# Kernel tuning notes

Hardware: AMD Instinct MI355X
Metric: run time of the kernel (lower is better)

The kernel has to match this reference:

```python
import jax, jax.numpy as jnp
import numpy as np

D_IN = 1024
D_OUT = 1024

def setup_inputs() -> dict:
    key = jax.random.key(0)
    ks = jax.random.split(key, 7)
    s = 1.0 / np.sqrt(D_IN)
    x = jax.random.normal(ks[0], (4, 2048, D_IN), dtype=jnp.float32)
    Wq = jax.random.uniform(ks[1], (D_IN, D_OUT), jnp.float32, -s, s)
    bq = jax.random.uniform(ks[2], (D_OUT,), jnp.float32, -s, s)
    Wk = jax.random.uniform(ks[3], (D_IN, D_OUT), jnp.float32, -s, s)
    bk = jax.random.uniform(ks[4], (D_OUT,), jnp.float32, -s, s)
    Wv = jax.random.uniform(ks[5], (D_IN, D_OUT), jnp.float32, -s, s)
    bv = jax.random.uniform(ks[6], (D_OUT,), jnp.float32, -s, s)
    return {"x": x, "Wq": Wq, "bq": bq, "Wk": Wk, "bk": bk, "Wv": Wv, "bv": bv}

def reference(x, Wq, bq, Wk, bk, Wv, bv):
    # q,k,v: [B, T, d_out]
    q = x @ Wq + bq
    k = x @ Wk + bk
    v = x @ Wv + bv
    T = x.shape[1]
    scale = 1.0 / jnp.sqrt(jnp.asarray(D_OUT, x.dtype))
    qk = jnp.einsum('btd,bsd->bts', q, k) * scale  # [B, T, T]
    causal = jnp.tril(jnp.ones((T, T), dtype=bool))
    qk = jnp.where(causal, qk, -jnp.inf)
    probs = jax.nn.softmax(qk, axis=-1)
    return jnp.einsum('bts,bsd->btd', probs, v)
```

## Files before the change

### kernel.cpp

```cpp
#include <hip/hip_runtime.h>
#include <cstdint>
#include <cmath>

#define D_MODEL 1024
#define SEQ 2048
#define BATCH 4

typedef short bf16x8 __attribute__((ext_vector_type(8)));
typedef float f32x4 __attribute__((ext_vector_type(4)));

__device__ __forceinline__ short f2bf(float f) {
  union { float f; unsigned int u; } v; v.f = f;
  unsigned int r = (v.u + 0x7FFFu + ((v.u >> 16) & 1u)) >> 16;
  return (short)r;
}

__device__ __forceinline__ float bf2f(short h) {
  union { unsigned int u; float f; } v;
  v.u = ((unsigned int)(unsigned short)h) << 16;
  return v.f;
}

__device__ __forceinline__ f32x4 mfma16(bf16x8 a, bf16x8 b, f32x4 c) {
  return __builtin_amdgcn_mfma_f32_16x16x32_bf16(a, b, c, 0, 0, 0);
}

__device__ __forceinline__ void load_lds16(const void* g, void* l) {
  __builtin_amdgcn_global_load_lds(
      (const __attribute__((address_space(1))) unsigned int*)g,
      (__attribute__((address_space(3))) unsigned int*)l, 16, 0, 0);
}

__global__ __launch_bounds__(256) void convert_x(const float* __restrict__ x,
                                                 short* __restrict__ xb) {
  int i = blockIdx.x * 256 + threadIdx.x;
  float4 f = ((const float4*)x)[i];
  short4 h;
  h.x = f2bf(f.x); h.y = f2bf(f.y); h.z = f2bf(f.z); h.w = f2bf(f.w);
  ((short4*)xb)[i] = h;
}

__global__ __launch_bounds__(256) void transpose_w(const float* __restrict__ Wq,
                                                   const float* __restrict__ Wk,
                                                   const float* __restrict__ Wv,
                                                   short* __restrict__ wt) {
  const int mat = blockIdx.z;
  const float* __restrict__ W = (mat == 0) ? Wq : (mat == 1) ? Wk : Wv;
  short* __restrict__ o = wt + (size_t)mat * (D_MODEL * D_MODEL);
  __shared__ float tile[32][33];
  const int k0 = blockIdx.x * 32, n0 = blockIdx.y * 32;
  const int lx = threadIdx.x & 31, ly = threadIdx.x >> 5;
#pragma unroll
  for (int i = 0; i < 4; ++i) {
    int r = ly + i * 8;
    tile[r][lx] = W[(size_t)(k0 + r) * D_MODEL + n0 + lx];
  }
  __syncthreads();
#pragma unroll
  for (int i = 0; i < 4; ++i) {
    int r = ly + i * 8;
    o[(size_t)(n0 + r) * D_MODEL + k0 + lx] = f2bf(tile[lx][r]);
  }
}

__global__ __launch_bounds__(256) void qkv_gemm(
    const short* __restrict__ xb, const short* __restrict__ wt,
    const float* __restrict__ bq, const float* __restrict__ bk,
    const float* __restrict__ bv, short* __restrict__ qo,
    short* __restrict__ ko, short* __restrict__ vo) {
  const int m0 = blockIdx.x * 128;
  const int n0 = blockIdx.y * 128;
  const int mat = blockIdx.z;
  const short* __restrict__ w = wt + (size_t)mat * (D_MODEL * D_MODEL);
  const float* __restrict__ bias = (mat == 0) ? bq : (mat == 1) ? bk : bv;

  __shared__ short a_lds[128 * 64];
  __shared__ short b_lds[128 * 64];

  const int tid = threadIdx.x;
  const int wid = tid >> 6;
  const int lane = tid & 63;
  const int quad = lane >> 4;
  const int l16 = lane & 15;
  const int mw = (wid >> 1) * 64;
  const int nw = (wid & 1) * 64;

  f32x4 acc[4][4] = {};

  const int r_local = wid * 8 + (lane >> 3);
  const int c_local = (lane & 7) * 8;

  for (int k0 = 0; k0 < D_MODEL; k0 += 64) {
    __syncthreads();
#pragma unroll
    for (int it = 0; it < 4; ++it) {
      const short* srcA = xb + (size_t)(m0 + it * 32 + r_local) * D_MODEL + k0 + c_local;
      load_lds16(srcA, (char*)a_lds + (it * 256 + wid * 64) * 16);
      const short* srcB = w + (size_t)(n0 + it * 32 + r_local) * D_MODEL + k0 + c_local;
      load_lds16(srcB, (char*)b_lds + (it * 256 + wid * 64) * 16);
    }
    __syncthreads();
#pragma unroll
    for (int kt = 0; kt < 2; ++kt) {
      bf16x8 af[4], bfr[4];
#pragma unroll
      for (int i = 0; i < 4; ++i)
        af[i] = *(const bf16x8*)(a_lds + (mw + i * 16 + l16) * 64 + kt * 32 + quad * 8);
#pragma unroll
      for (int i = 0; i < 4; ++i)
        bfr[i] = *(const bf16x8*)(b_lds + (nw + i * 16 + l16) * 64 + kt * 32 + quad * 8);
#pragma unroll
      for (int i = 0; i < 4; ++i)
#pragma unroll
        for (int j = 0; j < 4; ++j)
          acc[i][j] = mfma16(af[i], bfr[j], acc[i][j]);
    }
  }
#pragma unroll
  for (int i = 0; i < 4; ++i) {
#pragma unroll
    for (int j = 0; j < 4; ++j) {
#pragma unroll
      for (int r = 0; r < 4; ++r) {
        const int mrow = m0 + mw + i * 16 + quad * 4 + r;
        const int ncol = n0 + nw + j * 16 + l16;
        const float val = acc[i][j][r] + bias[ncol];
        const short h = f2bf(val);
        if (mat == 2) {
          const int bb = mrow >> 11;
          const int t = mrow & 2047;
          vo[((size_t)bb * D_MODEL + ncol) * SEQ + t] = h;
        } else if (mat == 0) {
          qo[(size_t)mrow * D_MODEL + ncol] = h;
        } else {
          ko[(size_t)mrow * D_MODEL + ncol] = h;
        }
      }
    }
  }
}

__global__ __launch_bounds__(256) void sgemm(const short* __restrict__ qb,
                                             const short* __restrict__ kb,
                                             short* __restrict__ S) {
  if (blockIdx.y > blockIdx.x) return;
  const int m0 = blockIdx.x * 128;
  const int n0 = blockIdx.y * 128;
  const int b = blockIdx.z;
  const short* __restrict__ qp = qb + (size_t)b * SEQ * D_MODEL;
  const short* __restrict__ kp = kb + (size_t)b * SEQ * D_MODEL;

  __shared__ short a_lds[128 * 64];
  __shared__ short b_lds[128 * 64];

  const int tid = threadIdx.x;
  const int wid = tid >> 6;
  const int lane = tid & 63;
  const int quad = lane >> 4;
  const int l16 = lane & 15;
  const int mw = (wid >> 1) * 64;
  const int nw = (wid & 1) * 64;

  f32x4 acc[4][4] = {};

  const int r_local = wid * 8 + (lane >> 3);
  const int c_local = (lane & 7) * 8;

  for (int k0 = 0; k0 < D_MODEL; k0 += 64) {
    __syncthreads();
#pragma unroll
    for (int it = 0; it < 4; ++it) {
      const short* srcA = qp + (size_t)(m0 + it * 32 + r_local) * D_MODEL + k0 + c_local;
      load_lds16(srcA, (char*)a_lds + (it * 256 + wid * 64) * 16);
      const short* srcB = kp + (size_t)(n0 + it * 32 + r_local) * D_MODEL + k0 + c_local;
      load_lds16(srcB, (char*)b_lds + (it * 256 + wid * 64) * 16);
    }
    __syncthreads();
#pragma unroll
    for (int kt = 0; kt < 2; ++kt) {
      bf16x8 af[4], bfr[4];
#pragma unroll
      for (int i = 0; i < 4; ++i)
        af[i] = *(const bf16x8*)(a_lds + (mw + i * 16 + l16) * 64 + kt * 32 + quad * 8);
#pragma unroll
      for (int i = 0; i < 4; ++i)
        bfr[i] = *(const bf16x8*)(b_lds + (nw + i * 16 + l16) * 64 + kt * 32 + quad * 8);
#pragma unroll
      for (int i = 0; i < 4; ++i)
#pragma unroll
        for (int j = 0; j < 4; ++j)
          acc[i][j] = mfma16(af[i], bfr[j], acc[i][j]);
    }
  }
#pragma unroll
  for (int i = 0; i < 4; ++i) {
#pragma unroll
    for (int j = 0; j < 4; ++j) {
#pragma unroll
      for (int r = 0; r < 4; ++r) {
        const int mrow = m0 + mw + i * 16 + quad * 4 + r;
        const int ncol = n0 + nw + j * 16 + l16;
        S[((size_t)b * SEQ + mrow) * SEQ + ncol] = f2bf(acc[i][j][r] * 0.03125f);
      }
    }
  }
}

__global__ __launch_bounds__(256) void softmax_rows(const short* __restrict__ S,
                                                    short* __restrict__ P) {
  const int row = blockIdx.x;
  const int t = row & (SEQ - 1);
  const int tid = threadIdx.x;
  const short* __restrict__ srow = S + (size_t)row * SEQ;
  short* __restrict__ prow = P + (size_t)row * SEQ;

  __shared__ float red[4];

  float v[8];
#pragma unroll
  for (int i = 0; i < 8; ++i) {
    const int c = tid + i * 256;
    v[i] = (c <= t) ? bf2f(srow[c]) : -1e30f;
  }
  float m = v[0];
#pragma unroll
  for (int i = 1; i < 8; ++i) m = fmaxf(m, v[i]);
#pragma unroll
  for (int o = 32; o; o >>= 1) m = fmaxf(m, __shfl_xor(m, o));
  if ((tid & 63) == 0) red[tid >> 6] = m;
  __syncthreads();
  m = fmaxf(fmaxf(red[0], red[1]), fmaxf(red[2], red[3]));

  float e[8];
  float s = 0.f;
#pragma unroll
  for (int i = 0; i < 8; ++i) {
    e[i] = __expf(v[i] - m);
    s += e[i];
  }
#pragma unroll
  for (int o = 32; o; o >>= 1) s += __shfl_xor(s, o);
  __syncthreads();
  if ((tid & 63) == 0) red[tid >> 6] = s;
  __syncthreads();
  s = red[0] + red[1] + red[2] + red[3];
  const float rinv = 1.0f / s;
#pragma unroll
  for (int i = 0; i < 8; ++i) prow[tid + i * 256] = f2bf(e[i] * rinv);
}

__global__ __launch_bounds__(256) void pvgemm(const short* __restrict__ P,
                                              const short* __restrict__ vtb,
                                              float* __restrict__ out) {
  const int m0 = blockIdx.x * 128;
  const int n0 = blockIdx.y * 128;
  const int b = blockIdx.z;
  const short* __restrict__ pp = P + (size_t)b * SEQ * SEQ;
  const short* __restrict__ vp = vtb + (size_t)b * D_MODEL * SEQ;
  const int kmax = m0 + 128;

  __shared__ short a_lds[128 * 64];
  __shared__ short b_lds[128 * 64];

  const int tid = threadIdx.x;
  const int wid = tid >> 6;
  const int lane = tid & 63;
  const int quad = lane >> 4;
  const int l16 = lane & 15;
  const int mw = (wid >> 1) * 64;
  const int nw = (wid & 1) * 64;

  f32x4 acc[4][4] = {};

  const int r_local = wid * 8 + (lane >> 3);
  const int c_local = (lane & 7) * 8;

  for (int k0 = 0; k0 < kmax; k0 += 64) {
    __syncthreads();
#pragma unroll
    for (int it = 0; it < 4; ++it) {
      const short* srcA = pp + (size_t)(m0 + it * 32 + r_local) * SEQ + k0 + c_local;
      load_lds16(srcA, (char*)a_lds + (it * 256 + wid * 64) * 16);
      const short* srcB = vp + (size_t)(n0 + it * 32 + r_local) * SEQ + k0 + c_local;
      load_lds16(srcB, (char*)b_lds + (it * 256 + wid * 64) * 16);
    }
    __syncthreads();
#pragma unroll
    for (int kt = 0; kt < 2; ++kt) {
      bf16x8 af[4], bfr[4];
#pragma unroll
      for (int i = 0; i < 4; ++i)
        af[i] = *(const bf16x8*)(a_lds + (mw + i * 16 + l16) * 64 + kt * 32 + quad * 8);
#pragma unroll
      for (int i = 0; i < 4; ++i)
        bfr[i] = *(const bf16x8*)(b_lds + (nw + i * 16 + l16) * 64 + kt * 32 + quad * 8);
#pragma unroll
      for (int i = 0; i < 4; ++i)
#pragma unroll
        for (int j = 0; j < 4; ++j)
          acc[i][j] = mfma16(af[i], bfr[j], acc[i][j]);
    }
  }
#pragma unroll
  for (int i = 0; i < 4; ++i) {
#pragma unroll
    for (int j = 0; j < 4; ++j) {
#pragma unroll
      for (int r = 0; r < 4; ++r) {
        const int mrow = m0 + mw + i * 16 + quad * 4 + r;
        const int ncol = n0 + nw + j * 16 + l16;
        out[((size_t)b * SEQ + mrow) * D_MODEL + ncol] = acc[i][j][r];
      }
    }
  }
}

extern "C" void kernel_launch(void* const* d_in, const int* in_sizes, int n_in,
                              void* d_out, int out_size, void* d_ws, size_t ws_size,
                              hipStream_t stream) {
  (void)in_sizes; (void)n_in; (void)out_size; (void)ws_size;
  const float* x  = (const float*)d_in[0];
  const float* Wq = (const float*)d_in[1];
  const float* bq = (const float*)d_in[2];
  const float* Wk = (const float*)d_in[3];
  const float* bk = (const float*)d_in[4];
  const float* Wv = (const float*)d_in[5];
  const float* bv = (const float*)d_in[6];
  float* out = (float*)d_out;

  char* ws = (char*)d_ws;
  short* xb = (short*)(ws);
  short* wt = (short*)(ws + 16777216);
  short* qo = (short*)(ws + 23068672);
  short* ko = (short*)(ws + 39845888);
  short* vo = (short*)(ws + 56623104);
  short* S  = (short*)(ws + 73400320);
  short* P  = (short*)(ws);

  convert_x<<<dim3(8192), dim3(256), 0, stream>>>(x, xb);
  transpose_w<<<dim3(32, 32, 3), dim3(256), 0, stream>>>(Wq, Wk, Wv, wt);
  qkv_gemm<<<dim3(64, 8, 3), dim3(256), 0, stream>>>(xb, wt, bq, bk, bv, qo, ko, vo);
  sgemm<<<dim3(16, 16, BATCH), dim3(256), 0, stream>>>(qo, ko, S);
  softmax_rows<<<dim3(BATCH * SEQ), dim3(256), 0, stream>>>(S, P);
  pvgemm<<<dim3(16, 8, BATCH), dim3(256), 0, stream>>>(P, vo, out);
}
```

Measured before the change: 304.9 us.

## Enlarge QKV GEMM tile, skip masked softmax stores, reorder PV grid heavy-first

```diff
diff --git a/kernel.cpp b/kernel.cpp
--- a/kernel.cpp
+++ b/kernel.cpp
@@ -63,18 +63,18 @@
   }
 }
 
-__global__ __launch_bounds__(256) void qkv_gemm(
+__global__ __launch_bounds__(512) void qkv_gemm(
     const short* __restrict__ xb, const short* __restrict__ wt,
     const float* __restrict__ bq, const float* __restrict__ bk,
     const float* __restrict__ bv, short* __restrict__ qo,
     short* __restrict__ ko, short* __restrict__ vo) {
-  const int m0 = blockIdx.x * 128;
+  const int m0 = blockIdx.x * 256;
   const int n0 = blockIdx.y * 128;
   const int mat = blockIdx.z;
   const short* __restrict__ w = wt + (size_t)mat * (D_MODEL * D_MODEL);
   const float* __restrict__ bias = (mat == 0) ? bq : (mat == 1) ? bk : bv;
 
-  __shared__ short a_lds[128 * 64];
+  __shared__ short a_lds[256 * 64];
   __shared__ short b_lds[128 * 64];
 
   const int tid = threadIdx.x;
@@ -82,8 +82,8 @@
   const int lane = tid & 63;
   const int quad = lane >> 4;
   const int l16 = lane & 15;
-  const int mw = (wid >> 1) * 64;
-  const int nw = (wid & 1) * 64;
+  const int wm = (wid >> 1) * 64;
+  const int wn = (wid & 1) * 64;
 
   f32x4 acc[4][4] = {};
 
@@ -94,10 +94,13 @@
     __syncthreads();
 #pragma unroll
     for (int it = 0; it < 4; ++it) {
-      const short* srcA = xb + (size_t)(m0 + it * 32 + r_local) * D_MODEL + k0 + c_local;
-      load_lds16(srcA, (char*)a_lds + (it * 256 + wid * 64) * 16);
-      const short* srcB = w + (size_t)(n0 + it * 32 + r_local) * D_MODEL + k0 + c_local;
-      load_lds16(srcB, (char*)b_lds + (it * 256 + wid * 64) * 16);
+      const short* srcA = xb + (size_t)(m0 + it * 64 + r_local) * D_MODEL + k0 + c_local;
+      load_lds16(srcA, (char*)a_lds + it * 8192 + wid * 1024);
+    }
+#pragma unroll
+    for (int it = 0; it < 2; ++it) {
+      const short* srcB = w + (size_t)(n0 + it * 64 + r_local) * D_MODEL + k0 + c_local;
+      load_lds16(srcB, (char*)b_lds + it * 8192 + wid * 1024);
     }
     __syncthreads();
 #pragma unroll
@@ -105,10 +108,10 @@
       bf16x8 af[4], bfr[4];
 #pragma unroll
       for (int i = 0; i < 4; ++i)
-        af[i] = *(const bf16x8*)(a_lds + (mw + i * 16 + l16) * 64 + kt * 32 + quad * 8);
-#pragma unroll
-      for (int i = 0; i < 4; ++i)
-        bfr[i] = *(const bf16x8*)(b_lds + (nw + i * 16 + l16) * 64 + kt * 32 + quad * 8);
+        af[i] = *(const bf16x8*)(a_lds + (wm + i * 16 + l16) * 64 + kt * 32 + quad * 8);
+#pragma unroll
+      for (int i = 0; i < 4; ++i)
+        bfr[i] = *(const bf16x8*)(b_lds + (wn + i * 16 + l16) * 64 + kt * 32 + quad * 8);
 #pragma unroll
       for (int i = 0; i < 4; ++i)
 #pragma unroll
@@ -122,8 +125,8 @@
     for (int j = 0; j < 4; ++j) {
 #pragma unroll
       for (int r = 0; r < 4; ++r) {
-        const int mrow = m0 + mw + i * 16 + quad * 4 + r;
-        const int ncol = n0 + nw + j * 16 + l16;
+        const int mrow = m0 + wm + i * 16 + quad * 4 + r;
+        const int ncol = n0 + wn + j * 16 + l16;
         const float val = acc[i][j][r] + bias[ncol];
         const short h = f2bf(val);
         if (mat == 2) {
@@ -245,16 +248,18 @@
   __syncthreads();
   s = red[0] + red[1] + red[2] + red[3];
   const float rinv = 1.0f / s;
-#pragma unroll
-  for (int i = 0; i < 8; ++i) prow[tid + i * 256] = f2bf(e[i] * rinv);
+  const int nwr = (t >> 8) + 1;
+#pragma unroll
+  for (int i = 0; i < 8; ++i)
+    if (i < nwr) prow[tid + i * 256] = f2bf(e[i] * rinv);
 }
 
 __global__ __launch_bounds__(256) void pvgemm(const short* __restrict__ P,
                                               const short* __restrict__ vtb,
                                               float* __restrict__ out) {
-  const int m0 = blockIdx.x * 128;
-  const int n0 = blockIdx.y * 128;
-  const int b = blockIdx.z;
+  const int n0 = blockIdx.x * 128;
+  const int b = blockIdx.y;
+  const int m0 = (15 - blockIdx.z) * 128;
   const short* __restrict__ pp = P + (size_t)b * SEQ * SEQ;
   const short* __restrict__ vp = vtb + (size_t)b * D_MODEL * SEQ;
   const int kmax = m0 + 128;
@@ -339,8 +344,8 @@
 
   convert_x<<<dim3(8192), dim3(256), 0, stream>>>(x, xb);
   transpose_w<<<dim3(32, 32, 3), dim3(256), 0, stream>>>(Wq, Wk, Wv, wt);
-  qkv_gemm<<<dim3(64, 8, 3), dim3(256), 0, stream>>>(xb, wt, bq, bk, bv, qo, ko, vo);
+  qkv_gemm<<<dim3(32, 8, 3), dim3(512), 0, stream>>>(xb, wt, bq, bk, bv, qo, ko, vo);
   sgemm<<<dim3(16, 16, BATCH), dim3(256), 0, stream>>>(qo, ko, S);
   softmax_rows<<<dim3(BATCH * SEQ), dim3(256), 0, stream>>>(S, P);
-  pvgemm<<<dim3(16, 8, BATCH), dim3(256), 0, stream>>>(P, vo, out);
-}
+  pvgemm<<<dim3(8, BATCH, 16), dim3(256), 0, stream>>>(P, vo, out);
+}
```

Measured after the change: 289.3 us. 1.05x faster.
